# Performance work log

Hardware: AMD Instinct MI355X
Metric: run time of the kernel (lower is better)

Reference implementation:

```python
import jax, jax.numpy as jnp
import numpy as np
import math

B, L, D = 8, 2048, 256
NUM_TYPES = 1
T_MAX = 200.0
SIGMA = 1.0


def setup_inputs() -> dict:
    key = jax.random.key(0)
    ks = jax.random.split(key, 12)
    event_type = jnp.ones((B, L), dtype=jnp.int64 if jax.config.jax_enable_x64 else jnp.int32)
    t = jax.random.uniform(ks[0], (B, L), dtype=jnp.float32) * T_MAX
    event_time = jnp.sort(t, axis=-1)
    s = 1.0 / math.sqrt(D)
    emb_weight = jax.random.normal(ks[1], (NUM_TYPES + 1, D), jnp.float32)
    emb_weight = emb_weight.at[0].set(0.0)  # padding_idx=0
    gate_w = jax.random.normal(ks[2], (2, D), jnp.float32) * s
    gate_b = jnp.zeros((2,), jnp.float32)
    ker_w = jax.random.normal(ks[3], (1, D), jnp.float32) * s
    ker_b = jnp.zeros((1,), jnp.float32)
    ln_gamma = jnp.ones((D,), jnp.float32)
    ln_beta = jnp.zeros((D,), jnp.float32)
    gen_input_w = jax.random.normal(ks[4], (D, D), jnp.float32) * s
    gen_noise_w = jax.random.normal(ks[5], (D, D), jnp.float32) * s
    gen_out_w = jax.random.normal(ks[6], (1, D), jnp.float32) * s
    gen_out_b = jnp.zeros((1,), jnp.float32)
    noise = jax.random.uniform(ks[7], (B, L, D), jnp.float32)  # torch.rand noise in Generator
    return dict(event_type=event_type, event_time=event_time, emb_weight=emb_weight,
                gate_w=gate_w, gate_b=gate_b, ker_w=ker_w, ker_b=ker_b,
                ln_gamma=ln_gamma, ln_beta=ln_beta, gen_input_w=gen_input_w,
                gen_noise_w=gen_noise_w, gen_out_w=gen_out_w, gen_out_b=gen_out_b,
                noise=noise)


def _softplus_beta(x, beta):
    return jax.nn.softplus(beta * x) / beta


def reference(event_type, event_time, emb_weight, gate_w, gate_b, ker_w, ker_b,
              ln_gamma, ln_beta, gen_input_w, gen_noise_w, gen_out_w, gen_out_b, noise):
    d_model = emb_weight.shape[-1]
    # ---- temporal positional encoding (this is `embedding`) ----
    pos_vec = jnp.power(10000.0, 2.0 * jnp.arange(d_model, dtype=jnp.float32) / d_model)
    t = event_time[:, :, None] / pos_vec                      # [B,L,D]
    idx = jnp.arange(d_model)
    temp_enc = jnp.where(idx % 2 == 0, jnp.sin(t), jnp.cos(t))
    # ---- type embedding ----
    te = emb_weight[event_type] * math.sqrt(d_model)          # [B,L,D]
    # ---- pairwise |t_i - t_j| ; xt[b,i,j]=t_i, xt_bar[b,i,j]=t_j ----
    dt = jnp.abs(event_time[:, :, None] - event_time[:, None, :])  # [B,L,L]
    # ---- squared exponential kernel: params depend only on row i (xd[b,i,j]=te[b,i]) ----
    ls = _softplus_beta(te @ ker_w.T + ker_b, 0.2)[..., 0]    # [B,L]
    scores_k = (SIGMA ** 2) * jnp.exp(-(dt ** 2) / (ls[:, :, None] ** 2))
    # ---- sigmoid gate ----
    p = jax.nn.sigmoid(te @ gate_w.T + gate_b)                # [B,L,2]
    l = p[..., 0][:, :, None]
    s = p[..., 1][:, :, None]
    gate = 1.0 + 0.5 * jnp.tanh((dt / T_MAX - l) / s)
    scores = scores_k * gate                                  # [B,L,L]
    # ---- causal mask: strictly-upper-triangle -> -1e10, then softmax ----
    causal = jnp.tril(jnp.ones((event_time.shape[1], event_time.shape[1]), jnp.bool_))
    scores = jnp.where(causal[None], scores, -1e10)
    attn = jax.nn.softmax(scores, axis=-1)
    # ---- hidden = attn @ temp_enc, layernorm ----
    hidden = jnp.einsum('bij,bjd->bid', attn, temp_enc)
    mu = hidden.mean(-1, keepdims=True)
    var = hidden.var(-1, keepdims=True)
    hidden = (hidden - mu) / jnp.sqrt(var + 1e-6) * ln_gamma + ln_beta
    # ---- Generator (dropout in eval = identity) ----
    h = jax.nn.relu(noise @ gen_noise_w.T + hidden @ gen_input_w.T)
    out = jax.nn.softplus(h @ gen_out_w.T + gen_out_b)[..., 0]  # [B,L]
    return out
```

## Files before the change

kernel.cpp:

```cpp
#include <hip/hip_runtime.h>
#include <hip/hip_bf16.h>

#define BD 8
#define LD 2048
#define DD 256
#define LOG2E 1.4426950408889634f

typedef unsigned short ushort_t;
typedef __attribute__((ext_vector_type(8))) short short8;
typedef __attribute__((ext_vector_type(4))) float floatx4;

__device__ __forceinline__ ushort_t f2bfu(float x) {
  __hip_bfloat16 h = __float2bfloat16(x);
  return *reinterpret_cast<ushort_t*>(&h);
}

__device__ __forceinline__ float exp2fast(float x) {
#if __has_builtin(__builtin_amdgcn_exp2f)
  return __builtin_amdgcn_exp2f(x);
#else
  return __expf(x * 0.6931471805599453f);
#endif
}

__device__ __forceinline__ void dma16(const ushort_t* g, ushort_t* l) {
  __builtin_amdgcn_global_load_lds(
      (const __attribute__((address_space(1))) unsigned int*)g,
      (__attribute__((address_space(3))) unsigned int*)l,
      16, 0, 0);
}

__device__ __forceinline__ float sin_acc(float a) {
  float k = rintf(a * 0.15915494f);
  float r = __builtin_fmaf(-k, 6.2831855f, a);
  r = __builtin_fmaf(-k, -1.7484555e-7f, r);
  return __sinf(r);
}
__device__ __forceinline__ float cos_acc(float a) {
  float k = rintf(a * 0.15915494f);
  float r = __builtin_fmaf(-k, 6.2831855f, a);
  r = __builtin_fmaf(-k, -1.7484555e-7f, r);
  return __cosf(r);
}

__device__ __forceinline__ short8 pk8(float4 a, float4 b) {
  short8 r;
  r[0] = (short)f2bfu(a.x); r[1] = (short)f2bfu(a.y);
  r[2] = (short)f2bfu(a.z); r[3] = (short)f2bfu(a.w);
  r[4] = (short)f2bfu(b.x); r[5] = (short)f2bfu(b.y);
  r[6] = (short)f2bfu(b.z); r[7] = (short)f2bfu(b.w);
  return r;
}

__global__ __launch_bounds__(256) void k_prep(
    const float* __restrict__ etime, const float* __restrict__ embw,
    const float* __restrict__ gatew, const float* __restrict__ gateb,
    const float* __restrict__ kerw, const float* __restrict__ kerb,
    const float* __restrict__ wn, const float* __restrict__ wi,
    ushort_t* __restrict__ enc_bf, ushort_t* __restrict__ wcat,
    float* __restrict__ ptable)
{
  const int bk = blockIdx.x;
  const int tid = threadIdx.x;
  __shared__ float ts[32];
  __shared__ float red[4][3];
  if (bk < 512) {
    if (tid < 32) ts[tid] = etime[(bk >> 6) * LD + (bk & 63) * 32 + tid];
    __syncthreads();
    uint4* dst = (uint4*)(enc_bf + (size_t)bk * 8192);
    const int jb = (tid & 3) * 8;
    #pragma unroll
    for (int jblk = 0; jblk < 4; ++jblk) {
      int d = jblk * 64 + (tid >> 2);
      float freq = __expf(-0.07195578416f * (float)d);
      unsigned int pk[4];
      #pragma unroll
      for (int p = 0; p < 4; ++p) {
        float a0 = ts[jb + 2 * p] * freq;
        float a1 = ts[jb + 2 * p + 1] * freq;
        float v0 = (d & 1) ? cos_acc(a0) : sin_acc(a0);
        float v1 = (d & 1) ? cos_acc(a1) : sin_acc(a1);
        pk[p] = (unsigned int)f2bfu(v0) | ((unsigned int)f2bfu(v1) << 16);
      }
      dst[jblk * 256 + tid] = make_uint4(pk[0], pk[1], pk[2], pk[3]);
    }
  } else if (bk < 640) {
    int p = (bk - 512) * 256 + tid;
    int c = p >> 7;
    int k = (p & 127) * 4;
    const float* src = (k < 256) ? (wn + c * 256 + k) : (wi + c * 256 + (k - 256));
    float4 f = *(const float4*)src;
    ushort4 u;
    u.x = f2bfu(f.x); u.y = f2bfu(f.y); u.z = f2bfu(f.z); u.w = f2bfu(f.w);
    *(ushort4*)(wcat + (size_t)c * 512 + k) = u;
  } else {
    int d = tid;
    int lane = d & 63, wvi = d >> 6;
    for (int ty = 0; ty < 2; ++ty) {
      float te = embw[ty * DD + d] * 16.0f;
      float p1 = te * kerw[d];
      float p2 = te * gatew[d];
      float p3 = te * gatew[DD + d];
      #pragma unroll
      for (int off = 32; off > 0; off >>= 1) {
        p1 += __shfl_xor(p1, off);
        p2 += __shfl_xor(p2, off);
        p3 += __shfl_xor(p3, off);
      }
      if (lane == 0) { red[wvi][0] = p1; red[wvi][1] = p2; red[wvi][2] = p3; }
      __syncthreads();
      if (d == 0) {
        float s1 = red[0][0] + red[1][0] + red[2][0] + red[3][0] + kerb[0];
        float s2 = red[0][1] + red[1][1] + red[2][1] + red[3][1] + gateb[0];
        float s3 = red[0][2] + red[1][2] + red[2][2] + red[3][2] + gateb[1];
        float z = 0.2f * s1;
        float sp = (z > 15.0f) ? z : log1pf(__expf(z));
        float ls = 5.0f * sp;
        float il = 1.0f / (ls * ls);
        float l  = 1.0f / (1.0f + __expf(-s2));
        float s  = 1.0f / (1.0f + __expf(-s3));
        float is2 = 2.0f / s;
        ptable[ty * 4 + 0] = -il * LOG2E;
        ptable[ty * 4 + 1] = 0.005f * is2 * LOG2E;
        ptable[ty * 4 + 2] = l * is2 * LOG2E;
      }
      __syncthreads();
    }
  }
}

__global__ __launch_bounds__(256, 2) void k_attn(
    const ushort_t* __restrict__ enc_bf, const float* __restrict__ etime,
    const int* __restrict__ etype, const float* __restrict__ ptable,
    const float* __restrict__ gamma, const float* __restrict__ beta,
    ushort_t* __restrict__ hidden_bf)
{
  __shared__ __align__(16) ushort_t stage[4][8192];
  const int tid = threadIdx.x;
  const int lane = tid & 63, wv = tid >> 6;
  const int bk = blockIdx.x;
  const int b = bk & 7;
  const int t64 = bk >> 3;
  const int g = (bk < 256) ? (63 - t64) : (t64 - 32);
  const int base = b * LD;
  const int m = lane & 15, kg = lane >> 4;
  const int i0 = g * 32 + m;
  const int i1 = i0 + 16;
  const float ti0 = etime[base + i0];
  const float ti1 = etime[base + i1];
  const int ty0 = etype[base + i0] * 4;
  const int ty1 = etype[base + i1] * 4;
  const float p00 = ptable[ty0 + 0], p01 = ptable[ty0 + 1], p02 = ptable[ty0 + 2];
  const float p10 = ptable[ty1 + 0], p11 = ptable[ty1 + 1], p12 = ptable[ty1 + 2];
  floatx4 acc0[16], acc1[16];
  #pragma unroll
  for (int nt = 0; nt < 16; ++nt) {
    acc0[nt] = (floatx4){0.f, 0.f, 0.f, 0.f};
    acc1[nt] = (floatx4){0.f, 0.f, 0.f, 0.f};
  }
  const int nch = g + 1;
  const ushort_t* __restrict__ encC = enc_bf + (size_t)(b * 64) * 8192;
  const int boff = m * 32 + kg * 8;
  ushort_t* mybuf = &stage[wv][0];

#define WPAIR(V, MASKED)                                                      \
  {                                                                           \
    float d0 = ti0 - tj[V];                                                   \
    float d1 = ti1 - tj[V];                                                   \
    float e10 = exp2fast(d0 * d0 * p00);                                      \
    float e11 = exp2fast(d1 * d1 * p10);                                      \
    float z0 = __builtin_fmaf(fabsf(d0), p01, -p02);                          \
    float z1 = __builtin_fmaf(fabsf(d1), p11, -p12);                          \
    float r0 = __builtin_amdgcn_rcpf(exp2fast(z0) + 1.0f);                    \
    float r1 = __builtin_amdgcn_rcpf(exp2fast(z1) + 1.0f);                    \
    float w0 = exp2fast(e10 * __builtin_fmaf(r0, -LOG2E, 1.5f * LOG2E));      \
    float w1 = exp2fast(e11 * __builtin_fmaf(r1, -LOG2E, 1.5f * LOG2E));      \
    if (MASKED) {                                                             \
      w0 = (j0 + V <= i0) ? w0 : 0.0f;                                        \
      w1 = (j0 + V <= i1) ? w1 : 0.0f;                                        \
    }                                                                         \
    af0[V] = (short)f2bfu(w0);                                                \
    af1[V] = (short)f2bfu(w1);                                                \
  }

  for (int ch = wv; ch < nch; ch += 4) {
    const int j0 = ch * 32 + kg * 8;
    float4 tja = *(const float4*)(etime + base + j0);
    float4 tjb = *(const float4*)(etime + base + j0 + 4);
    __builtin_amdgcn_s_waitcnt(0xC07F);
    const ushort_t* gsrc = encC + (size_t)ch * 8192 + lane * 8;
    #pragma unroll
    for (int nt = 0; nt < 16; ++nt)
      dma16(gsrc + nt * 512, mybuf + nt * 512);
    float tj[8] = {tja.x, tja.y, tja.z, tja.w, tjb.x, tjb.y, tjb.z, tjb.w};
    short8 af0, af1;
    if (ch < g) {
      #pragma unroll
      for (int v = 0; v < 8; ++v) WPAIR(v, false)
    } else {
      #pragma unroll
      for (int v = 0; v < 8; ++v) WPAIR(v, true)
    }
    __builtin_amdgcn_s_waitcnt(0x0F70);
    #pragma unroll
    for (int nt = 0; nt < 16; ++nt) {
      short8 bf = *(const short8*)(mybuf + nt * 512 + boff);
      acc0[nt] = __builtin_amdgcn_mfma_f32_16x16x32_bf16(af0, bf, acc0[nt], 0, 0, 0);
      acc1[nt] = __builtin_amdgcn_mfma_f32_16x16x32_bf16(af1, bf, acc1[nt], 0, 0, 0);
    }
  }
#undef WPAIR

  __syncthreads();
  floatx4* lacc = (floatx4*)&stage[0][0];
  if (wv != 0) {
    #pragma unroll
    for (int nt = 0; nt < 16; ++nt) lacc[((wv - 1) * 16 + nt) * 64 + lane] = acc0[nt];
  }
  __syncthreads();
  if (wv == 0) {
    #pragma unroll
    for (int nt = 0; nt < 16; ++nt)
      acc0[nt] = acc0[nt] + lacc[nt * 64 + lane]
                          + lacc[(16 + nt) * 64 + lane]
                          + lacc[(32 + nt) * 64 + lane];
  }
  __syncthreads();
  if (wv != 1) {
    const int widx = (wv == 0) ? 0 : (wv - 1);
    #pragma unroll
    for (int nt = 0; nt < 16; ++nt) lacc[(widx * 16 + nt) * 64 + lane] = acc1[nt];
  }
  __syncthreads();
  if (wv == 1) {
    #pragma unroll
    for (int nt = 0; nt < 16; ++nt)
      acc0[nt] = acc1[nt] + lacc[nt * 64 + lane]
                          + lacc[(16 + nt) * 64 + lane]
                          + lacc[(32 + nt) * 64 + lane];
  }
  if (wv < 2) {
    float gl[16], cl[16];
    #pragma unroll
    for (int nt = 0; nt < 16; ++nt) { gl[nt] = gamma[nt * 16 + m]; cl[nt] = beta[nt * 16 + m]; }
    const int q = lane >> 4;
    const int row0 = base + g * 32 + wv * 16;
    #pragma unroll
    for (int r = 0; r < 4; ++r) {
      float h[16];
      float sm = 0.0f, sq = 0.0f;
      #pragma unroll
      for (int nt = 0; nt < 16; ++nt) {
        h[nt] = acc0[nt][r];
        sm += h[nt]; sq += h[nt] * h[nt];
      }
      #pragma unroll
      for (int off = 1; off < 16; off <<= 1) {
        sm += __shfl_xor(sm, off);
        sq += __shfl_xor(sq, off);
      }
      float mean = sm * (1.0f / 256.0f);
      float var = sq * (1.0f / 256.0f) - mean * mean;
      float rstd = rsqrtf(var + 1e-6f);
      ushort_t* dst = hidden_bf + ((size_t)(row0 + q * 4 + r)) * DD + m;
      #pragma unroll
      for (int nt = 0; nt < 16; ++nt)
        dst[nt * 16] = f2bfu((h[nt] - mean) * rstd * gl[nt] + cl[nt]);
    }
  }
}

__global__ __launch_bounds__(256) void k_gen(
    const float* __restrict__ noise, const ushort_t* __restrict__ hidden_bf,
    const ushort_t* __restrict__ wcat, const float* __restrict__ wout,
    const float* __restrict__ bout, float* __restrict__ out)
{
  __shared__ float pbuf[4][2][16];
  const int tid = threadIdx.x;
  const int lane = tid & 63, wv = tid >> 6;
  const int m = lane & 15, kg = lane >> 4;
  const int r0 = blockIdx.x * 32 + m;
  const float* __restrict__ nf0 = noise + (size_t)r0 * DD;
  const float* __restrict__ nf1 = noise + (size_t)(r0 + 16) * DD;
  const ushort_t* __restrict__ ah0 = hidden_bf + (size_t)r0 * DD;
  const ushort_t* __restrict__ ah1 = hidden_bf + (size_t)(r0 + 16) * DD;
  floatx4 acc[2][4];
  #pragma unroll
  for (int t = 0; t < 2; ++t)
    #pragma unroll
    for (int n = 0; n < 4; ++n) acc[t][n] = (floatx4){0.f, 0.f, 0.f, 0.f};
  const ushort_t* __restrict__ bbase = wcat + ((size_t)(wv * 4) * 16 + m) * 512 + kg * 8;
  #pragma unroll
  for (int ks = 0; ks < 16; ++ks) {
    const int koff = (ks & 7) * 32 + kg * 8;
    short8 a0, a1;
    if (ks < 8) {
      float4 fa = *(const float4*)(nf0 + koff);
      float4 fb = *(const float4*)(nf0 + koff + 4);
      a0 = pk8(fa, fb);
      fa = *(const float4*)(nf1 + koff);
      fb = *(const float4*)(nf1 + koff + 4);
      a1 = pk8(fa, fb);
    } else {
      a0 = *(const short8*)(ah0 + koff);
      a1 = *(const short8*)(ah1 + koff);
    }
    const ushort_t* bp = bbase + ks * 32;
    #pragma unroll
    for (int n = 0; n < 4; ++n) {
      short8 bf = *(const short8*)(bp + (size_t)n * 8192);
      acc[0][n] = __builtin_amdgcn_mfma_f32_16x16x32_bf16(a0, bf, acc[0][n], 0, 0, 0);
      acc[1][n] = __builtin_amdgcn_mfma_f32_16x16x32_bf16(a1, bf, acc[1][n], 0, 0, 0);
    }
  }
  float wo_l[4];
  #pragma unroll
  for (int n = 0; n < 4; ++n) wo_l[n] = wout[(wv * 4 + n) * 16 + m];
  #pragma unroll
  for (int t = 0; t < 2; ++t) {
    #pragma unroll
    for (int r4 = 0; r4 < 4; ++r4) {
      float p = 0.0f;
      #pragma unroll
      for (int n = 0; n < 4; ++n) p += fmaxf(acc[t][n][r4], 0.0f) * wo_l[n];
      #pragma unroll
      for (int off = 1; off < 16; off <<= 1) p += __shfl_xor(p, off);
      if (m == 0) pbuf[wv][t][kg * 4 + r4] = p;
    }
  }
  __syncthreads();
  if (tid < 32) {
    int t = tid >> 4, rr = tid & 15;
    float x = pbuf[0][t][rr] + pbuf[1][t][rr] + pbuf[2][t][rr] + pbuf[3][t][rr] + bout[0];
    float sp = (x > 15.0f) ? x : log1pf(__expf(x));
    out[blockIdx.x * 32 + t * 16 + rr] = sp;
  }
}

extern "C" void kernel_launch(void* const* d_in, const int* in_sizes, int n_in,
                              void* d_out, int out_size, void* d_ws, size_t ws_size,
                              hipStream_t stream) {
  const int*   etype = (const int*)d_in[0];
  const float* etime = (const float*)d_in[1];
  const float* embw  = (const float*)d_in[2];
  const float* gatew = (const float*)d_in[3];
  const float* gateb = (const float*)d_in[4];
  const float* kerw  = (const float*)d_in[5];
  const float* kerb  = (const float*)d_in[6];
  const float* gamma = (const float*)d_in[7];
  const float* beta  = (const float*)d_in[8];
  const float* wi    = (const float*)d_in[9];
  const float* wn    = (const float*)d_in[10];
  const float* wo    = (const float*)d_in[11];
  const float* bo    = (const float*)d_in[12];
  const float* noise = (const float*)d_in[13];
  float* out = (float*)d_out;

  char* w8 = (char*)d_ws;
  float* ptable       = (float*)(w8);
  ushort_t* enc_bf    = (ushort_t*)(w8 + 262144);
  ushort_t* hidden_bf = (ushort_t*)(w8 + 262144 + 8388608);
  ushort_t* wcat      = (ushort_t*)(w8 + 262144 + 2 * 8388608);

  k_prep<<<641, 256, 0, stream>>>(etime, embw, gatew, gateb, kerw, kerb,
                                  wn, wi, enc_bf, wcat, ptable);
  k_attn<<<512, 256, 0, stream>>>(enc_bf, etime, etype, ptable,
                                  gamma, beta, hidden_bf);
  k_gen<<<512, 256, 0, stream>>>(noise, hidden_bf, wcat, wo, bo, out);
}
```

Measured before the change: 148.9 us.

## Pair causal row tiles per 512-thread block and pre-swizzle encoding for linear LDS reads

Each attention block now has 8 waves and handles two row tiles, g and 63-g, so every block carries the same total causal work. The previous scheme sent tiles to separate blocks in long-first order. The encoding prep kernel now writes its bf16 tiles in the MFMA B-operand order, so each lane reads LDS at lane*8 with no strided offset. The cost is double the LDS per block (128 KB), which may limit residency to one block per CU. The reduction and layernorm paths are also duplicated across the two wave groups.

```diff
diff --git a/kernel.cpp b/kernel.cpp
--- a/kernel.cpp
+++ b/kernel.cpp
@@ -68,10 +68,11 @@
     if (tid < 32) ts[tid] = etime[(bk >> 6) * LD + (bk & 63) * 32 + tid];
     __syncthreads();
     uint4* dst = (uint4*)(enc_bf + (size_t)bk * 8192);
-    const int jb = (tid & 3) * 8;
     #pragma unroll
     for (int jblk = 0; jblk < 4; ++jblk) {
-      int d = jblk * 64 + (tid >> 2);
+      const int idx4 = jblk * 256 + tid;
+      const int d = ((idx4 >> 6) << 4) | (idx4 & 15);
+      const int jb = ((idx4 >> 4) & 3) * 8;
       float freq = __expf(-0.07195578416f * (float)d);
       unsigned int pk[4];
       #pragma unroll
@@ -82,7 +83,7 @@
         float v1 = (d & 1) ? cos_acc(a1) : sin_acc(a1);
         pk[p] = (unsigned int)f2bfu(v0) | ((unsigned int)f2bfu(v1) << 16);
       }
-      dst[jblk * 256 + tid] = make_uint4(pk[0], pk[1], pk[2], pk[3]);
+      dst[idx4] = make_uint4(pk[0], pk[1], pk[2], pk[3]);
     }
   } else if (bk < 640) {
     int p = (bk - 512) * 256 + tid;
@@ -129,22 +130,23 @@
   }
 }
 
-__global__ __launch_bounds__(256, 2) void k_attn(
+__global__ __launch_bounds__(512, 2) void k_attn(
     const ushort_t* __restrict__ enc_bf, const float* __restrict__ etime,
     const int* __restrict__ etype, const float* __restrict__ ptable,
     const float* __restrict__ gamma, const float* __restrict__ beta,
     ushort_t* __restrict__ hidden_bf)
 {
-  __shared__ __align__(16) ushort_t stage[4][8192];
+  __shared__ __align__(16) ushort_t stage[8][8192];
   const int tid = threadIdx.x;
   const int lane = tid & 63, wv = tid >> 6;
   const int bk = blockIdx.x;
   const int b = bk & 7;
-  const int t64 = bk >> 3;
-  const int g = (bk < 256) ? (63 - t64) : (t64 - 32);
+  const int idx = bk >> 3;
+  const int myg = (wv < 4) ? (63 - idx) : idx;
+  const int kwv = wv & 3;
   const int base = b * LD;
   const int m = lane & 15, kg = lane >> 4;
-  const int i0 = g * 32 + m;
+  const int i0 = myg * 32 + m;
   const int i1 = i0 + 16;
   const float ti0 = etime[base + i0];
   const float ti1 = etime[base + i1];
@@ -158,9 +160,8 @@
     acc0[nt] = (floatx4){0.f, 0.f, 0.f, 0.f};
     acc1[nt] = (floatx4){0.f, 0.f, 0.f, 0.f};
   }
-  const int nch = g + 1;
+  const int nch = myg + 1;
   const ushort_t* __restrict__ encC = enc_bf + (size_t)(b * 64) * 8192;
-  const int boff = m * 32 + kg * 8;
   ushort_t* mybuf = &stage[wv][0];
 
 #define WPAIR(V, MASKED)                                                      \
@@ -183,7 +184,7 @@
     af1[V] = (short)f2bfu(w1);                                                \
   }
 
-  for (int ch = wv; ch < nch; ch += 4) {
+  for (int ch = kwv; ch < nch; ch += 4) {
     const int j0 = ch * 32 + kg * 8;
     float4 tja = *(const float4*)(etime + base + j0);
     float4 tjb = *(const float4*)(etime + base + j0 + 4);
@@ -194,7 +195,7 @@
       dma16(gsrc + nt * 512, mybuf + nt * 512);
     float tj[8] = {tja.x, tja.y, tja.z, tja.w, tjb.x, tjb.y, tjb.z, tjb.w};
     short8 af0, af1;
-    if (ch < g) {
+    if (ch < myg) {
       #pragma unroll
       for (int v = 0; v < 8; ++v) WPAIR(v, false)
     } else {
@@ -204,7 +205,7 @@
     __builtin_amdgcn_s_waitcnt(0x0F70);
     #pragma unroll
     for (int nt = 0; nt < 16; ++nt) {
-      short8 bf = *(const short8*)(mybuf + nt * 512 + boff);
+      short8 bf = *(const short8*)(mybuf + nt * 512 + lane * 8);
       acc0[nt] = __builtin_amdgcn_mfma_f32_16x16x32_bf16(af0, bf, acc0[nt], 0, 0, 0);
       acc1[nt] = __builtin_amdgcn_mfma_f32_16x16x32_bf16(af1, bf, acc1[nt], 0, 0, 0);
     }
@@ -213,38 +214,41 @@
 
   __syncthreads();
   floatx4* lacc = (floatx4*)&stage[0][0];
-  if (wv != 0) {
-    #pragma unroll
-    for (int nt = 0; nt < 16; ++nt) lacc[((wv - 1) * 16 + nt) * 64 + lane] = acc0[nt];
-  }
-  __syncthreads();
-  if (wv == 0) {
+  if (wv != 0 && wv != 4) {
+    const int slot = (wv < 4) ? (wv - 1) : (wv - 2);
+    #pragma unroll
+    for (int nt = 0; nt < 16; ++nt) lacc[(slot * 16 + nt) * 64 + lane] = acc0[nt];
+  }
+  __syncthreads();
+  if (wv == 0 || wv == 4) {
+    const int s0 = (wv == 0) ? 0 : 3;
     #pragma unroll
     for (int nt = 0; nt < 16; ++nt)
-      acc0[nt] = acc0[nt] + lacc[nt * 64 + lane]
-                          + lacc[(16 + nt) * 64 + lane]
-                          + lacc[(32 + nt) * 64 + lane];
-  }
-  __syncthreads();
-  if (wv != 1) {
-    const int widx = (wv == 0) ? 0 : (wv - 1);
-    #pragma unroll
-    for (int nt = 0; nt < 16; ++nt) lacc[(widx * 16 + nt) * 64 + lane] = acc1[nt];
-  }
-  __syncthreads();
-  if (wv == 1) {
+      acc0[nt] = acc0[nt] + lacc[((s0 + 0) * 16 + nt) * 64 + lane]
+                          + lacc[((s0 + 1) * 16 + nt) * 64 + lane]
+                          + lacc[((s0 + 2) * 16 + nt) * 64 + lane];
+  }
+  __syncthreads();
+  if (wv != 1 && wv != 5) {
+    const int slot = (wv < 4) ? ((wv == 0) ? 0 : (wv - 1)) : ((wv == 4) ? 3 : (wv - 2));
+    #pragma unroll
+    for (int nt = 0; nt < 16; ++nt) lacc[(slot * 16 + nt) * 64 + lane] = acc1[nt];
+  }
+  __syncthreads();
+  if (wv == 1 || wv == 5) {
+    const int s0 = (wv == 1) ? 0 : 3;
     #pragma unroll
     for (int nt = 0; nt < 16; ++nt)
-      acc0[nt] = acc1[nt] + lacc[nt * 64 + lane]
-                          + lacc[(16 + nt) * 64 + lane]
-                          + lacc[(32 + nt) * 64 + lane];
-  }
-  if (wv < 2) {
+      acc0[nt] = acc1[nt] + lacc[((s0 + 0) * 16 + nt) * 64 + lane]
+                          + lacc[((s0 + 1) * 16 + nt) * 64 + lane]
+                          + lacc[((s0 + 2) * 16 + nt) * 64 + lane];
+  }
+  if (wv == 0 || wv == 1 || wv == 4 || wv == 5) {
     float gl[16], cl[16];
     #pragma unroll
     for (int nt = 0; nt < 16; ++nt) { gl[nt] = gamma[nt * 16 + m]; cl[nt] = beta[nt * 16 + m]; }
-    const int q = lane >> 4;
-    const int row0 = base + g * 32 + wv * 16;
+    const int G = (wv < 4) ? (63 - idx) : idx;
+    const int row0 = base + G * 32 + (wv & 1) * 16;
     #pragma unroll
     for (int r = 0; r < 4; ++r) {
       float h[16];
@@ -262,7 +266,7 @@
       float mean = sm * (1.0f / 256.0f);
       float var = sq * (1.0f / 256.0f) - mean * mean;
       float rstd = rsqrtf(var + 1e-6f);
-      ushort_t* dst = hidden_bf + ((size_t)(row0 + q * 4 + r)) * DD + m;
+      ushort_t* dst = hidden_bf + ((size_t)(row0 + kg * 4 + r)) * DD + m;
       #pragma unroll
       for (int nt = 0; nt < 16; ++nt)
         dst[nt * 16] = f2bfu((h[nt] - mean) * rstd * gl[nt] + cl[nt]);
@@ -364,7 +368,7 @@
 
   k_prep<<<641, 256, 0, stream>>>(etime, embw, gatew, gateb, kerw, kerb,
                                   wn, wi, enc_bf, wcat, ptable);
-  k_attn<<<512, 256, 0, stream>>>(enc_bf, etime, etype, ptable,
+  k_attn<<<256, 512, 0, stream>>>(enc_bf, etime, etype, ptable,
                                   gamma, beta, hidden_bf);
   k_gen<<<512, 256, 0, stream>>>(noise, hidden_bf, wcat, wo, bo, out);
 }
```

New measurement: 149.2 us, median of 2. Within noise of the previous version (+0.1%).
